# Kernel tuning notes

Measured on AMD Instinct MI355X. Metric: run time of the kernel, lower is better.

## Reference

```python
import jax, jax.numpy as jnp
import numpy as np

B = 64        # graphs per batch
H = 8         # heads
EH = 16       # each_head = ceil(128/8)
HD = 128      # h_dimension
N_DA = 100000
N_Q = 20000
E_DA = 1000000
E_Q = 200000
EPS = 1e-5    # BatchNorm1d eps
SLOPE = 2.0   # leaky_relu_GAT_rate


def setup_inputs() -> dict:
    key = jax.random.key(0)
    ks = jax.random.split(key, 24)
    r = lambda i, shape, s=1.0: jax.random.normal(ks[i], shape, dtype=jnp.float32) * s
    return {
        'h_da_last': r(0, (N_DA, HD)),
        'h_q_last': r(1, (N_Q, HD)),
        'h_da_0': r(2, (N_DA, HD)),
        'h_q_0': r(3, (N_Q, HD)),
        'W_L': r(4, (HD, HD), 0.05), 'b_L': jnp.zeros((HD,), jnp.float32),
        'gateq_W': r(5, (HD, 1), 0.05), 'gateq_b': jnp.zeros((1,), jnp.float32),
        'gate1_W': r(6, (HD, 1), 0.05), 'gate1_b': jnp.zeros((1,), jnp.float32),
        'gate2_W': r(7, (HD, 1), 0.05), 'gate2_b': jnp.zeros((1,), jnp.float32),
        'Q_comb': r(8, (1, HD), 0.1),
        'Qf_W1': r(9, (HD, 2 * HD), 0.05), 'Qf_b1': jnp.zeros((2 * HD,), jnp.float32),
        'Qf_W2': r(10, (2 * HD, 2 * H * EH), 0.05), 'Qf_b2': jnp.zeros((2 * H * EH,), jnp.float32),
        'end_W1': r(11, (H * EH, 2 * HD), 0.05), 'end_b1': jnp.zeros((2 * HD,), jnp.float32),
        'end_W2': r(12, (2 * HD, HD), 0.05), 'end_b2': jnp.zeros((HD,), jnp.float32),
        'src_da': jax.random.randint(ks[13], (E_DA,), 0, N_DA),
        'dst_da': jax.random.randint(ks[14], (E_DA,), 0, N_DA),
        'src_q': jax.random.randint(ks[15], (E_Q,), 0, N_Q),
        'dst_q': jax.random.randint(ks[16], (E_Q,), 0, N_Q),
        'gid_da': jnp.sort(jax.random.randint(ks[17], (N_DA,), 0, B)),
        'gid_q': jnp.sort(jax.random.randint(ks[18], (N_Q,), 0, B)),
        'PEid': jax.random.randint(ks[19], (100000,), 0, E_DA),
        'DEid': jax.random.randint(ks[20], (100000,), 0, E_DA),
        'len_Mn': 5,
    }


def _bn(y):
    # BatchNorm1d(affine=False), training mode: biased batch stats
    mu = jnp.mean(y, axis=0)
    var = jnp.mean((y - mu) ** 2, axis=0)
    return (y - mu) / jnp.sqrt(var + EPS)


def _fnn(x, W1, b1, W2, b2):
    y = jax.nn.elu(_bn(x @ W1 + b1))
    return jax.nn.elu(_bn(y @ W2 + b2))


def _gap(W, b, feat, gid):
    # GlobalAttentionPooling: softmax(gate) over nodes per graph, weighted sum
    g = (feat @ W + b)[:, 0]                               # [N]
    m = jax.ops.segment_max(g, gid, num_segments=B)
    e = jnp.exp(g - m[gid])
    s = jax.ops.segment_sum(e, gid, num_segments=B)
    w = e / s[gid]
    return jax.ops.segment_sum(w[:, None] * feat, gid, num_segments=B)  # [B, HD]


def _edge_softmax(e, dst, n):
    # softmax over incoming edges per destination node, per head. e: [E, H, 1]
    m = jax.ops.segment_max(e, dst, num_segments=n)
    ex = jnp.exp(e - m[dst])
    s = jax.ops.segment_sum(ex, dst, num_segments=n)
    return ex / s[dst]


def forward(h_da_last, h_q_last, h_da_0, h_q_0, W_L, b_L, gateq_W, gateq_b,
            gate1_W, gate1_b, gate2_W, gate2_b, Q_comb, Qf_W1, Qf_b1, Qf_W2, Qf_b2,
            end_W1, end_b1, end_W2, end_b2,
            src_da, dst_da, src_q, dst_q, gid_da, gid_q, PEid, DEid, len_Mn):
    tmp_q = h_q_last  # MM is None branch

    # graph-level query representation -> per-graph attention queries Q [B, H, 2*EH]
    glq = _gap(gateq_W, gateq_b, h_q_last, gid_q)
    Q = _fnn(glq, Qf_W1, Qf_b1, Qf_W2, Qf_b2).reshape(B, H, 2 * EH)

    def att_comb(M1, M2, gid):
        # ATTpolling_for_3Dtensor with shared Q_comb
        k1 = _gap(gate1_W, gate1_b, M1, gid)
        k2 = _gap(gate2_W, gate2_b, M2, gid)
        s = jnp.stack([(Q_comb * k1).sum(-1), (Q_comb * k2).sum(-1)], axis=-1)  # [B, 2]
        a = jax.nn.softmax(s, axis=-1)[gid]                                     # [N, 2]
        return M1 * a[:, 0:1] + M2 * a[:, 1:2]

    def branch(h_last, tmp, h0, M2, src, dst, gid, n):
        Qn = Q[gid]                                  # [n, H, 2*EH]
        Ql, Qr = Qn[..., :EH], Qn[..., EH:]
        feat = (tmp @ W_L + b_L).reshape(n, H, EH)
        el = (feat * Ql).sum(-1, keepdims=True)      # [n, H, 1]
        er = (feat * Qr).sum(-1, keepdims=True)
        fh = att_comb(h0, M2, gid)
        ft = (fh @ W_L + b_L).reshape(n, H, EH)
        e = jax.nn.leaky_relu(el[src] + er[dst], negative_slope=SLOPE)  # [E, H, 1]
        a = _edge_softmax(e, dst, n)
        agg = jax.ops.segment_sum(ft[src] * a, dst, num_segments=n)     # [n, H, EH]
        out = _fnn(agg.reshape(n, H * EH), end_W1, end_b1, end_W2, end_b2)
        return h_last + out, a                       # residual=True

    h_q_next, _ = branch(h_q_last, tmp_q, h_q_0, h_q_last + (h_q_last - tmp_q),
                         src_q, dst_q, gid_q, N_Q)
    h_da_next, a_da = branch(h_da_last, h_da_last, h_da_0, h_da_last,
                             src_da, dst_da, gid_da, N_DA)

    PE = a_da[PEid].sum(axis=0)                      # [H, 1]
    DE = a_da[DEid].sum(axis=0)
    loss = -1.0 * jnp.mean((PE - DE) / len_Mn, axis=0).reshape(1, 1)
    return h_da_next, h_q_next, loss


def reference(h_da_last, h_q_last, h_da_0, h_q_0, W_L, b_L, gateq_W, gateq_b,
              gate1_W, gate1_b, gate2_W, gate2_b, Q_comb, Qf_W1, Qf_b1, Qf_W2, Qf_b2,
              end_W1, end_b1, end_W2, end_b2,
              src_da, dst_da, src_q, dst_q, gid_da, gid_q, PEid, DEid, len_Mn):
    return forward(h_da_last, h_q_last, h_da_0, h_q_0, W_L, b_L, gateq_W, gateq_b,
                   gate1_W, gate1_b, gate2_W, gate2_b, Q_comb, Qf_W1, Qf_b1, Qf_W2, Qf_b2,
                   end_W1, end_b1, end_W2, end_b2,
                   src_da, dst_da, src_q, dst_q, gid_da, gid_q, PEid, DEid, len_Mn)
```

## Files before the change

kernel.cpp:

```cpp
#include <hip/hip_runtime.h>
#include <math.h>

static constexpr int CB   = 64;
static constexpr int CH   = 8;
static constexpr int CEH  = 16;
static constexpr int CHD  = 128;
static constexpr int CNDA = 100000;
static constexpr int CNQ  = 20000;
static constexpr int CEDA = 1000000;
static constexpr int CEQ  = 200000;
static constexpr float CEPS = 1e-5f;
static constexpr float CSLOPE = 2.0f;

typedef unsigned short ushortt;
typedef __attribute__((ext_vector_type(8))) short bf16x8;
typedef __attribute__((ext_vector_type(4))) float f32x4;

__device__ __forceinline__ float ldf(const float* p) { return *p; }
__device__ __forceinline__ float ldf(const ushortt* p) {
  return __uint_as_float(((unsigned)*p) << 16);
}
__device__ __forceinline__ void stf(float* p, float v) { *p = v; }
__device__ __forceinline__ void stf(ushortt* p, float v) {
  unsigned u = __float_as_uint(v);
  u += 0x7fff + ((u >> 16) & 1);
  *p = (ushortt)(u >> 16);
}
__device__ __forceinline__ short f2bf(float v) {
  unsigned u = __float_as_uint(v);
  u += 0x7fff + ((u >> 16) & 1);
  return (short)(u >> 16);
}
__device__ __forceinline__ float bf2f(short b) {
  return __uint_as_float(((unsigned)(ushortt)b) << 16);
}
__device__ __forceinline__ unsigned fenc(float f) {
  unsigned b = __float_as_uint(f);
  return (b & 0x80000000u) ? ~b : (b | 0x80000000u);
}
__device__ __forceinline__ float fdec(unsigned u) {
  unsigned b = (u & 0x80000000u) ? (u ^ 0x80000000u) : ~u;
  return __uint_as_float(b);
}

__global__ void k_zero(float* __restrict__ p, long n) {
  long i = (long)blockIdx.x * blockDim.x + threadIdx.x;
  long stride = (long)gridDim.x * blockDim.x;
  for (; i < n; i += stride) p[i] = 0.f;
}
static inline void zero_launch(void* p, long n, hipStream_t s) {
  long b = (n + 255) / 256;
  int blocks = (int)(b > 4096 ? 4096 : (b < 1 ? 1 : b));
  hipLaunchKernelGGL(k_zero, dim3(blocks), dim3(256), 0, s, (float*)p, n);
}

__global__ void k_binit(int* start, int n) {
  int i = threadIdx.x;
  if (i <= CB) start[i] = n;
}
__global__ void k_bmark(const int* __restrict__ gid, int n, int* __restrict__ start) {
  int i = blockIdx.x * blockDim.x + threadIdx.x;
  if (i >= n) return;
  int g = gid[i];
  if (i == 0 || gid[i - 1] != g) atomicMin(&start[g], i);
}
__global__ void k_bfix(int* start) {
  if (threadIdx.x == 0) {
    for (int g = CB - 1; g >= 0; --g)
      if (start[g] > start[g + 1]) start[g] = start[g + 1];
  }
}

__global__ void k_gate_dot(const float* __restrict__ feat, const float* __restrict__ gw,
                           const float* __restrict__ gb, float* __restrict__ g, int n) {
  int wave = (blockIdx.x * blockDim.x + threadIdx.x) >> 6;
  int lane = threadIdx.x & 63;
  if (wave >= n) return;
  const float* row = feat + (size_t)wave * CHD;
  float v = row[lane] * gw[lane] + row[lane + 64] * gw[lane + 64];
  for (int off = 32; off > 0; off >>= 1) v += __shfl_down(v, off, 64);
  if (lane == 0) g[wave] = v + gb[0];
}

__global__ void k_gate_dot2(const float* __restrict__ feat,
                            const float* __restrict__ w1, const float* __restrict__ b1,
                            const float* __restrict__ w2, const float* __restrict__ b2,
                            float* __restrict__ g1, float* __restrict__ g2, int n) {
  int wave = (blockIdx.x * blockDim.x + threadIdx.x) >> 6;
  int lane = threadIdx.x & 63;
  if (wave >= n) return;
  const float* row = feat + (size_t)wave * CHD;
  float r0 = row[lane], r1 = row[lane + 64];
  float v1 = r0 * w1[lane] + r1 * w1[lane + 64];
  float v2 = r0 * w2[lane] + r1 * w2[lane + 64];
  for (int off = 32; off > 0; off >>= 1) {
    v1 += __shfl_down(v1, off, 64);
    v2 += __shfl_down(v2, off, 64);
  }
  if (lane == 0) {
    g1[wave] = v1 + b1[0];
    g2[wave] = v2 + b2[0];
  }
}

__global__ void k_gmax5(const float* __restrict__ gq, const int* __restrict__ startq,
                        const int* __restrict__ startda, float* __restrict__ m) {
  int job = blockIdx.x >> 6, grp = blockIdx.x & 63;
  const float* g;
  const int* start;
  if (job == 0)      { g = gq;                              start = startq; }
  else if (job == 1) { g = gq + 2 * (size_t)CNQ;            start = startq; }
  else if (job == 2) { g = gq + (size_t)CNQ;                start = startq; }
  else if (job == 3) { g = gq + 3 * (size_t)CNQ;            start = startda; }
  else               { g = gq + 3 * (size_t)CNQ + CNDA;     start = startda; }
  int s0 = start[grp], s1 = start[grp + 1];
  int t = threadIdx.x;
  __shared__ float red[256];
  float v = -1e30f;
  for (int i = s0 + t; i < s1; i += 256) v = fmaxf(v, g[i]);
  red[t] = v;
  __syncthreads();
  for (int o = 128; o > 0; o >>= 1) {
    if (t < o) red[t] = fmaxf(red[t], red[t + o]);
    __syncthreads();
  }
  if (t == 0) m[job * 64 + grp] = red[0];
}

template <int NG>
__global__ __launch_bounds__(128) void k_gap_partial(
    const float* __restrict__ g0, const float* __restrict__ g1,
    const float* __restrict__ feat, const int* __restrict__ start,
    const float* __restrict__ m,
    float* __restrict__ acc0, float* __restrict__ acc1,
    float* __restrict__ sums) {
  int grp = blockIdx.x;
  int s0 = start[grp], s1 = start[grp + 1];
  int len = s1 - s0;
  if (len <= 0) return;
  int NC = gridDim.y;
  int per = (len + NC - 1) / NC;
  int r0 = s0 + blockIdx.y * per;
  int r1 = min(s1, r0 + per);
  if (r0 >= r1) return;
  int t = threadIdx.x;
  float m0 = m[grp];
  float m1 = (NG == 2) ? m[64 + grp] : 0.f;
  float a0 = 0.f, a1 = 0.f, sum0 = 0.f, sum1 = 0.f;
  for (int i = r0; i < r1; ++i) {
    float f = feat[(size_t)i * CHD + t];
    float e0 = __expf(g0[i] - m0);
    sum0 += e0;
    a0 += e0 * f;
    if (NG == 2) {
      float e1 = __expf(g1[i] - m1);
      sum1 += e1;
      a1 += e1 * f;
    }
  }
  atomicAdd(&acc0[grp * CHD + t], a0);
  if (NG == 2) atomicAdd(&acc1[grp * CHD + t], a1);
  if (t == 0) {
    atomicAdd(&sums[grp], sum0);
    if (NG == 2) atomicAdd(&sums[64 + grp], sum1);
  }
}

__global__ void k_gap_norm5(float* __restrict__ glq, const float* __restrict__ sbuf) {
  int job = blockIdx.x >> 6, grp = blockIdx.x & 63;
  int t = threadIdx.x;
  int smap = (job == 1) ? 2 : ((job == 2) ? 1 : job);
  float sv = sbuf[smap * 64 + grp];
  float* acc = glq + (size_t)job * CB * CHD + grp * CHD;
  float v = acc[t];
  acc[t] = (sv > 0.f) ? v / sv : 0.f;
}

__global__ void k_mm_small(const float* __restrict__ X, const float* __restrict__ W,
                           const float* __restrict__ bias, float* __restrict__ Y,
                           int m, int k, int p) {
  int idx = blockIdx.x * blockDim.x + threadIdx.x;
  if (idx >= m * p) return;
  int r = idx / p, c = idx % p;
  const float* xr = X + (size_t)r * k;
  const float* wc = W + c;
  float acc = bias[c];
  int kk = 0;
  for (; kk + 8 <= k; kk += 8) {
    float xv[8], wv[8];
#pragma unroll
    for (int j = 0; j < 8; ++j) {
      xv[j] = xr[kk + j];
      wv[j] = wc[(size_t)(kk + j) * p];
    }
#pragma unroll
    for (int j = 0; j < 8; ++j) acc += xv[j] * wv[j];
  }
  for (; kk < k; ++kk) acc += xr[kk] * wc[(size_t)kk * p];
  Y[idx] = acc;
}

__global__ void k_bn_elu_small(float* __restrict__ Y, int m, int p) {
  int c = blockIdx.x * blockDim.x + threadIdx.x;
  if (c >= p) return;
  float s = 0.f, s2 = 0.f;
  int i = 0;
  for (; i + 8 <= m; i += 8) {
    float v[8];
#pragma unroll
    for (int j = 0; j < 8; ++j) v[j] = Y[(size_t)(i + j) * p + c];
#pragma unroll
    for (int j = 0; j < 8; ++j) { s += v[j]; s2 += v[j] * v[j]; }
  }
  for (; i < m; ++i) {
    float v = Y[(size_t)i * p + c];
    s += v; s2 += v * v;
  }
  float mu = s / m;
  float var = s2 / m - mu * mu;
  float inv = rsqrtf(var + CEPS);
  i = 0;
  for (; i + 8 <= m; i += 8) {
    float v[8];
#pragma unroll
    for (int j = 0; j < 8; ++j) v[j] = Y[(size_t)(i + j) * p + c];
#pragma unroll
    for (int j = 0; j < 8; ++j) {
      float x = (v[j] - mu) * inv;
      Y[(size_t)(i + j) * p + c] = x > 0.f ? x : expm1f(x);
    }
  }
  for (; i < m; ++i) {
    float x = (Y[(size_t)i * p + c] - mu) * inv;
    Y[(size_t)i * p + c] = x > 0.f ? x : expm1f(x);
  }
}

__global__ void k_attcomb(const float* __restrict__ k1, const float* __restrict__ k2,
                          const float* __restrict__ Qc, float* __restrict__ a) {
  int grp = blockIdx.x;
  int t = threadIdx.x;
  float v1 = Qc[t] * k1[grp * CHD + t] + Qc[t + 64] * k1[grp * CHD + t + 64];
  float v2 = Qc[t] * k2[grp * CHD + t] + Qc[t + 64] * k2[grp * CHD + t + 64];
  for (int off = 32; off > 0; off >>= 1) {
    v1 += __shfl_down(v1, off, 64);
    v2 += __shfl_down(v2, off, 64);
  }
  if (t == 0) {
    float mx = fmaxf(v1, v2);
    float e1 = expf(v1 - mx), e2 = expf(v2 - mx);
    float s = e1 + e2;
    a[grp * 2] = e1 / s;
    a[grp * 2 + 1] = e2 / s;
  }
}

__global__ void k_wq(const float* __restrict__ W_L, const float* __restrict__ b_L,
                     const float* __restrict__ Qm, float* __restrict__ WQ,
                     float* __restrict__ bQ) {
  int g = blockIdx.x;
  int t = threadIdx.x;
  for (int j = 0; j < 8; ++j) {
    int idx = t + j * 256;
    int d = idx >> 4, c = idx & 15;
    int h = c & 7, off = (c >= 8) ? CEH : 0;
    const float* w = W_L + d * CHD + h * CEH;
    const float* q = Qm + g * 256 + h * 32 + off;
    float acc = 0.f;
#pragma unroll
    for (int e = 0; e < CEH; ++e) acc += w[e] * q[e];
    WQ[g * 2048 + idx] = acc;
  }
  if (t < 16) {
    int c = t, h = c & 7, off = (c >= 8) ? CEH : 0;
    const float* b = b_L + h * CEH;
    const float* q = Qm + g * 256 + h * 32 + off;
    float acc = 0.f;
#pragma unroll
    for (int e = 0; e < CEH; ++e) acc += b[e] * q[e];
    bQ[g * 16 + c] = acc;
  }
}

__global__ void k_eler(const float* __restrict__ tmp, const float* __restrict__ WQ,
                       const float* __restrict__ bQ, const int* __restrict__ gid,
                       float* __restrict__ elr, int n) {
  int idx = blockIdx.x * blockDim.x + threadIdx.x;
  if (idx >= n * 16) return;
  int i = idx >> 4, c = idx & 15;
  int g = gid[i];
  const float* wq = WQ + g * 2048 + c;
  const float* row = tmp + (size_t)i * CHD;
  float acc = bQ[g * 16 + c];
#pragma unroll 4
  for (int d = 0; d < CHD; ++d) acc += row[d] * wq[d * 16];
  elr[idx] = acc;
}

__global__ void k_elmax(const float* __restrict__ elr, unsigned* __restrict__ mgl, int n) {
  int h = blockIdx.x;
  int chunk = blockIdx.y;
  int per = (n + 31) / 32;
  int i0 = chunk * per, i1 = min(n, i0 + per);
  int t = threadIdx.x;
  __shared__ float red[256];
  float v = -1e30f;
  for (int i = i0 + t; i < i1; i += 256) v = fmaxf(v, elr[(size_t)i * 16 + h]);
  red[t] = v;
  __syncthreads();
  for (int o = 128; o > 0; o >>= 1) {
    if (t < o) red[t] = fmaxf(red[t], red[t + o]);
    __syncthreads();
  }
  if (t == 0) atomicMax(&mgl[h], fenc(red[0]));
}

__global__ void k_tcast(const float* __restrict__ W, ushortt* __restrict__ WT,
                        int K, int P) {
  int i = blockIdx.x * blockDim.x + threadIdx.x;
  if (i >= K * P) return;
  int p = i / K, k = i % K;
  stf(&WT[i], W[(size_t)k * P + p]);
}

template <int P>
__global__ void k_bn_prep(const float* __restrict__ stats, float* __restrict__ pr, int n) {
  int c = threadIdx.x;
  if (c >= P) return;
  float invn = 1.f / (float)n;
  float mu = stats[c] * invn;
  float var = stats[P + c] * invn - mu * mu;
  pr[c] = mu;
  pr[P + c] = rsqrtf(var + CEPS);
}

template <int TP>
__global__ void k_stats_reduce(const float* __restrict__ pstat, float* __restrict__ stats,
                               int nb) {
  int c = blockIdx.x * blockDim.x + threadIdx.x;
  if (c >= TP) return;
  int NC = gridDim.y;
  int per = (nb + NC - 1) / NC;
  int r0 = blockIdx.y * per;
  int r1 = min(nb, r0 + per);
  if (r0 >= r1) return;
  float s0 = 0.f, s1 = 0.f, s2 = 0.f, s3 = 0.f;
  int r = r0;
  for (; r + 4 <= r1; r += 4) {
    s0 += pstat[(size_t)(r + 0) * TP + c];
    s1 += pstat[(size_t)(r + 1) * TP + c];
    s2 += pstat[(size_t)(r + 2) * TP + c];
    s3 += pstat[(size_t)(r + 3) * TP + c];
  }
  for (; r < r1; ++r) s0 += pstat[(size_t)r * TP + c];
  atomicAdd(&stats[c], (s0 + s1) + (s2 + s3));
}

template <int K, int P, int XM, bool STATS, int ROWS, bool LDSB, typename OT>
__global__ __launch_bounds__(256, 2) void k_gemm_mfma(
    const void* __restrict__ X0v, const void* __restrict__ X1v,
    const float* __restrict__ acomb, const int* __restrict__ gid,
    const float* __restrict__ bnpr, const ushortt* __restrict__ BT,
    const float* __restrict__ bias, OT* __restrict__ Y,
    float* __restrict__ pstat, int n) {
  constexpr int NT = P / 16;
  __shared__ ushortt sB[LDSB ? P * K : 1];
  __shared__ float sbn[(XM == 3) ? 2 * K : 1];
  if constexpr (XM == 3) {
    for (int i = threadIdx.x; i < 2 * K; i += 256) sbn[i] = bnpr[i];
  }
  if constexpr (LDSB) {
    for (int i = threadIdx.x; i < P * (K / 8); i += 256) {
      int row = i / (K / 8), seg = i % (K / 8);
      int sseg = seg ^ (row & 7);
      *(bf16x8*)&sB[row * K + sseg * 8] =
          *(const bf16x8*)(BT + (size_t)row * K + seg * 8);
    }
  }
  if constexpr (XM == 3 || LDSB) __syncthreads();
  const int wave = threadIdx.x >> 6, lane = threadIdx.x & 63;
  const int quad = lane >> 4, l16 = lane & 15;
  const int rbase = blockIdx.x * (64 * ROWS) + wave * 16;
  int rA[ROWS];
  bool rok[ROWS];
  float a0[ROWS], a1[ROWS];
#pragma unroll
  for (int rr = 0; rr < ROWS; ++rr) {
    rA[rr] = rbase + rr * 64 + l16;
    rok[rr] = rA[rr] < n;
    a0[rr] = 0.f; a1[rr] = 0.f;
    if (XM == 1 && rok[rr]) {
      int g = gid[rA[rr]];
      a0[rr] = acomb[2 * g];
      a1[rr] = acomb[2 * g + 1];
    }
  }
  f32x4 acc[ROWS][NT];
#pragma unroll
  for (int rr = 0; rr < ROWS; ++rr)
#pragma unroll
    for (int t = 0; t < NT; ++t) acc[rr][t] = f32x4{0.f, 0.f, 0.f, 0.f};
  for (int k0 = 0; k0 < K; k0 += 32) {
    const int kk = k0 + quad * 8;
    bf16x8 af[ROWS];
#pragma unroll
    for (int rr = 0; rr < ROWS; ++rr) {
      af[rr] = bf16x8{};
      if (rok[rr]) {
        if constexpr (XM == 2) {
          af[rr] = *(const bf16x8*)((const ushortt*)X0v + (size_t)rA[rr] * K + kk);
        } else if constexpr (XM == 3) {
          bf16x8 raw = *(const bf16x8*)((const ushortt*)X0v + (size_t)rA[rr] * K + kk);
#pragma unroll
          for (int j = 0; j < 8; ++j) {
            float v = bf2f(raw[j]);
            v = (v - sbn[kk + j]) * sbn[K + kk + j];
            v = v > 0.f ? v : (__expf(v) - 1.f);
            af[rr][j] = f2bf(v);
          }
        } else {
          const float* px = (const float*)X0v + (size_t)rA[rr] * K + kk;
          float v[8];
          if constexpr (XM == 1) {
            const float* py = (const float*)X1v + (size_t)rA[rr] * K + kk;
#pragma unroll
            for (int j = 0; j < 8; ++j) v[j] = a0[rr] * px[j] + a1[rr] * py[j];
          } else {
#pragma unroll
            for (int j = 0; j < 8; ++j) v[j] = px[j];
          }
#pragma unroll
          for (int j = 0; j < 8; ++j) af[rr][j] = f2bf(v[j]);
        }
      }
    }
    bf16x8 bfr[NT];
#pragma unroll
    for (int t = 0; t < NT; ++t) {
      if constexpr (LDSB) {
        int row = t * 16 + l16;
        int sseg = (kk >> 3) ^ (row & 7);
        bfr[t] = *(const bf16x8*)&sB[row * K + sseg * 8];
      } else {
        bfr[t] = *(const bf16x8*)(BT + (size_t)(t * 16 + l16) * K + kk);
      }
    }
#pragma unroll
    for (int rr = 0; rr < ROWS; ++rr)
#pragma unroll
      for (int t = 0; t < NT; ++t)
        acc[rr][t] = __builtin_amdgcn_mfma_f32_16x16x32_bf16(af[rr], bfr[t], acc[rr][t], 0, 0, 0);
  }
  float* pw = nullptr;
  if constexpr (STATS) pw = pstat + ((size_t)blockIdx.x * 4 + wave) * (2 * P);
#pragma unroll
  for (int t = 0; t < NT; ++t) {
    const int c = t * 16 + l16;
    float b = bias[c];
    float s = 0.f, s2 = 0.f;
#pragma unroll
    for (int rr = 0; rr < ROWS; ++rr) {
#pragma unroll
      for (int r = 0; r < 4; ++r) {
        int gr = rbase + rr * 64 + quad * 4 + r;
        if (gr < n) {
          float val = acc[rr][t][r] + b;
          stf(Y + (size_t)gr * P + c, val);
          if constexpr (STATS) {
            float vq = (sizeof(OT) == 2) ? bf2f(f2bf(val)) : val;
            s += vq;
            s2 += vq * vq;
          }
        }
      }
    }
    if constexpr (STATS) {
      s += __shfl_xor(s, 16, 64);
      s += __shfl_xor(s, 32, 64);
      s2 += __shfl_xor(s2, 16, 64);
      s2 += __shfl_xor(s2, 32, 64);
      if (quad == 0) {
        pw[c] = s;
        pw[P + c] = s2;
      }
    }
  }
}

__global__ void k_count(const int* __restrict__ dst, int* __restrict__ counts, int E) {
  int e = blockIdx.x * blockDim.x + threadIdx.x;
  if (e < E) atomicAdd(&counts[dst[e]], 1);
}
__global__ void k_scan_reduce(const int* __restrict__ counts, int* __restrict__ bsum, int n) {
  __shared__ int red[256];
  int t = threadIdx.x;
  int base = blockIdx.x * 1024;
  int s = 0;
  for (int j = 0; j < 4; ++j) {
    int i = base + t * 4 + j;
    if (i < n) s += counts[i];
  }
  red[t] = s;
  __syncthreads();
  for (int o = 128; o > 0; o >>= 1) {
    if (t < o) red[t] += red[t + o];
    __syncthreads();
  }
  if (t == 0) bsum[blockIdx.x] = red[0];
}
__global__ void k_scan_top(int* __restrict__ bsum, int nb) {
  __shared__ int sh[128];
  int t = threadIdx.x;
  int v = (t < nb) ? bsum[t] : 0;
  sh[t] = v;
  __syncthreads();
  for (int o = 1; o < 128; o <<= 1) {
    int x = (t >= o) ? sh[t - o] : 0;
    __syncthreads();
    sh[t] += x;
    __syncthreads();
  }
  if (t < nb) bsum[t] = sh[t] - v;
}
__global__ void k_scan_final(const int* __restrict__ counts, const int* __restrict__ bsum,
                             int* __restrict__ rowptr, int n, int E) {
  __shared__ int sh[256];
  int t = threadIdx.x;
  int base = blockIdx.x * 1024;
  int v[4];
  int s = 0;
  for (int j = 0; j < 4; ++j) {
    int i = base + t * 4 + j;
    v[j] = (i < n) ? counts[i] : 0;
    s += v[j];
  }
  sh[t] = s;
  __syncthreads();
  for (int o = 1; o < 256; o <<= 1) {
    int x = (t >= o) ? sh[t - o] : 0;
    __syncthreads();
    sh[t] += x;
    __syncthreads();
  }
  int off = bsum[blockIdx.x] + sh[t] - s;
  for (int j = 0; j < 4; ++j) {
    int i = base + t * 4 + j;
    if (i < n) rowptr[i] = off;
    off += v[j];
  }
  if (blockIdx.x == 0 && t == 0) rowptr[n] = E;
}
__global__ void k_copy_int(const int* __restrict__ a, int* __restrict__ b, int n) {
  int i = blockIdx.x * blockDim.x + threadIdx.x;
  if (i < n) b[i] = a[i];
}
__global__ void k_scatter(const int* __restrict__ dst, const int* __restrict__ srcA,
                          int* __restrict__ cursor, int* __restrict__ csr_src, int E) {
  int e = blockIdx.x * blockDim.x + threadIdx.x;
  if (e >= E) return;
  int d = dst[e];
  int pos = atomicAdd(&cursor[d], 1);
  csr_src[pos] = srcA[e];
}

__global__ __launch_bounds__(256) void k_node_agg(
    const int* __restrict__ rowptr, const int* __restrict__ csr_src,
    const float* __restrict__ elr, const unsigned* __restrict__ mgl,
    const ushortt* __restrict__ ft,
    float* __restrict__ agg, float* __restrict__ mOut, float* __restrict__ sOut, int n) {
  int node = blockIdx.x * 4 + (threadIdx.x >> 6);
  if (node >= n) return;
  int lane = threadIdx.x & 63;
  int h_p = lane & 7;
  int e_loc = lane >> 3;
  int h_a = lane >> 3;
  int s0 = rowptr[node], s1 = rowptr[node + 1];
  if (s1 <= s0) {
    *(float2*)(agg + (size_t)node * CHD + lane * 2) = make_float2(0.f, 0.f);
    if (lane < 8) {
      mOut[(size_t)node * CH + lane] = -1e30f;
      sOut[(size_t)node * CH + lane] = 0.f;
    }
    return;
  }
  float erd_p = elr[(size_t)node * 16 + 8 + h_p];
  float xm = fdec(mgl[h_p]) + erd_p;
  float m_p = xm >= 0.f ? xm : CSLOPE * xm;
  float s_part = 0.f, a0 = 0.f, a1 = 0.f;
  for (int base = s0; base < s1; base += 8) {
    int cnt = s1 - base;
    int sj = 0;
    float p = 0.f;
    if (e_loc < cnt) {
      sj = csr_src[base + e_loc];
      float x = elr[(size_t)sj * 16 + h_p] + erd_p;
      x = x >= 0.f ? x : CSLOPE * x;
      p = __expf(x - m_p);
      s_part += p;
    }
#pragma unroll
    for (int e = 0; e < 8; ++e) {
      float pe = __shfl(p, e * 8 + h_a, 64);
      int se = __shfl(sj, e * 8, 64);
      unsigned ftv = *(const unsigned*)(ft + (size_t)se * CHD + lane * 2);
      a0 += pe * __uint_as_float(ftv << 16);
      a1 += pe * __uint_as_float(ftv & 0xffff0000u);
    }
  }
  s_part += __shfl_xor(s_part, 8, 64);
  s_part += __shfl_xor(s_part, 16, 64);
  s_part += __shfl_xor(s_part, 32, 64);
  float s_acc = __shfl(s_part, h_a, 64);
  float inv = 1.f / s_acc;
  float2 o;
  o.x = a0 * inv;
  o.y = a1 * inv;
  *(float2*)(agg + (size_t)node * CHD + lane * 2) = o;
  if (lane < 8) {
    mOut[(size_t)node * CH + lane] = m_p;
    sOut[(size_t)node * CH + lane] = s_part;
  }
}

__global__ void k_bn_apply_f4(float* __restrict__ Y, const float* __restrict__ stats,
                              const float* __restrict__ hlast, int n) {
  int idx = blockIdx.x * blockDim.x + threadIdx.x;
  if (idx >= n * 32) return;
  int cg = (idx & 31) * 4;
  float invn = 1.f / (float)n;
  float4 y = ((const float4*)Y)[idx];
  float4 hl = ((const float4*)hlast)[idx];
  float yy[4] = {y.x, y.y, y.z, y.w};
  float hh[4] = {hl.x, hl.y, hl.z, hl.w};
  float o[4];
#pragma unroll
  for (int j = 0; j < 4; ++j) {
    float mu = stats[cg + j] * invn;
    float var = stats[128 + cg + j] * invn - mu * mu;
    float v = (yy[j] - mu) * rsqrtf(var + CEPS);
    v = v > 0.f ? v : (__expf(v) - 1.f);
    o[j] = v + hh[j];
  }
  ((float4*)Y)[idx] = make_float4(o[0], o[1], o[2], o[3]);
}

__device__ __forceinline__ float attn_val(int e, int h, const int* __restrict__ src,
                                          const int* __restrict__ dst,
                                          const float* __restrict__ elr,
                                          const float* __restrict__ mOut,
                                          const float* __restrict__ sOut) {
  int ss = src[e], sd = dst[e];
  float x = elr[(size_t)ss * 16 + h] + elr[(size_t)sd * 16 + 8 + h];
  x = x >= 0.f ? x : CSLOPE * x;
  return __expf(x - mOut[(size_t)sd * CH + h]) / sOut[(size_t)sd * CH + h];
}

__global__ void k_pd(const int* __restrict__ src, const int* __restrict__ dst,
                     const float* __restrict__ elr, const float* __restrict__ mOut,
                     const float* __restrict__ sOut, const int* __restrict__ PEid,
                     const int* __restrict__ DEid, float* __restrict__ pdp,
                     int nPE, int nDE) {
  __shared__ float part[CH];
  if (threadIdx.x < CH) part[threadIdx.x] = 0.f;
  __syncthreads();
  int idx = blockIdx.x * blockDim.x + threadIdx.x;
  int j = idx >> 3, h = idx & 7;
  float acc = 0.f;
  if (j < nPE) acc += attn_val(PEid[j], h, src, dst, elr, mOut, sOut);
  if (j < nDE) acc -= attn_val(DEid[j], h, src, dst, elr, mOut, sOut);
  atomicAdd(&part[h], acc);
  __syncthreads();
  if (threadIdx.x < CH) pdp[(size_t)blockIdx.x * CH + threadIdx.x] = part[threadIdx.x];
}
__global__ void k_loss(const float* __restrict__ pdp, int nb,
                       const int* __restrict__ lenMn, float* __restrict__ out) {
  __shared__ float part[CH];
  int t = threadIdx.x;
  if (t < CH) part[t] = 0.f;
  __syncthreads();
  int h = t & 7;
  float acc = 0.f;
  for (int j = t >> 3; j < nb; j += 32) acc += pdp[(size_t)j * CH + h];
  atomicAdd(&part[h], acc);
  __syncthreads();
  if (t == 0) {
    float len = (float)lenMn[0];
    float s = 0.f;
    for (int hh = 0; hh < CH; ++hh) s += part[hh] / len;
    out[0] = -s / (float)CH;
  }
}

static void run_branch(int n, int E, const float* h_last, const float* h0,
                       const int* src, const int* dst, const int* gid,
                       const float* acomb, const float* WQ, const float* bQ,
                       const ushortt* W_LT, const float* b_L,
                       const ushortt* W1T, const float* end_b1,
                       const ushortt* W2T, const float* end_b2,
                       float* U, float* elr, unsigned* mgl, float* mOut, float* sOut,
                       int* counts, int* rowptr, int* cursor, int* csr_src, int* bsum,
                       float* stats ,
                       float* bnpr , float* pstat, float* out, hipStream_t stream) {
  ushortt* ftB = (ushortt*)U;
  ushortt* y1B = (ushortt*)U;
  float* stats1 = stats;
  float* stats2 = stats + 512;
  int nChunks = (n + 1023) / 1024;
  int nbG1 = (n + 127) / 128;
  int nbG2 = (n + 63) / 64;
  zero_launch(counts, n, stream);
  zero_launch(stats, 1024, stream);
  zero_launch(mgl, 8, stream);
  hipLaunchKernelGGL(k_count, dim3((E + 255) / 256), dim3(256), 0, stream, dst, counts, E);
  hipLaunchKernelGGL(k_scan_reduce, dim3(nChunks), dim3(256), 0, stream, counts, bsum, n);
  hipLaunchKernelGGL(k_scan_top, dim3(1), dim3(128), 0, stream, bsum, nChunks);
  hipLaunchKernelGGL(k_scan_final, dim3(nChunks), dim3(256), 0, stream, counts, bsum, rowptr, n, E);
  hipLaunchKernelGGL(k_copy_int, dim3((n + 255) / 256), dim3(256), 0, stream, rowptr, cursor, n);
  hipLaunchKernelGGL(k_scatter, dim3((E + 255) / 256), dim3(256), 0, stream, dst, src, cursor, csr_src, E);
  hipLaunchKernelGGL(k_eler, dim3((n * 16 + 255) / 256), dim3(256), 0, stream,
                     h_last, WQ, bQ, gid, elr, n);
  hipLaunchKernelGGL(k_elmax, dim3(8, 32), dim3(256), 0, stream, elr, mgl, n);
  hipLaunchKernelGGL((k_gemm_mfma<128, 128, 1, false, 2, false, ushortt>), dim3(nbG1),
                     dim3(256), 0, stream, h0, h_last, acomb, gid,
                     (const float*)nullptr, W_LT, b_L, ftB, (float*)nullptr, n);
  hipLaunchKernelGGL(k_node_agg, dim3((n + 3) / 4), dim3(256), 0, stream,
                     rowptr, csr_src, elr, mgl, ftB, out, mOut, sOut, n);
  hipLaunchKernelGGL((k_gemm_mfma<128, 256, 0, true, 1, true, ushortt>), dim3(nbG2),
                     dim3(256), 0, stream, out, (const void*)nullptr,
                     (const float*)nullptr, (const int*)nullptr,
                     (const float*)nullptr, W1T, end_b1, y1B, pstat, n);
  hipLaunchKernelGGL((k_stats_reduce<512>), dim3(2, 64), dim3(256), 0, stream,
                     pstat, stats1, nbG2 * 4);
  hipLaunchKernelGGL((k_bn_prep<256>), dim3(1), dim3(256), 0, stream, stats1, bnpr, n);
  hipLaunchKernelGGL((k_gemm_mfma<256, 128, 3, true, 2, false, float>), dim3(nbG1),
                     dim3(256), 0, stream, y1B, (const void*)nullptr,
                     (const float*)nullptr, (const int*)nullptr,
                     bnpr, W2T, end_b2, out, pstat, n);
  hipLaunchKernelGGL((k_stats_reduce<256>), dim3(1, 64), dim3(256), 0, stream,
                     pstat, stats2, nbG1 * 4);
  hipLaunchKernelGGL(k_bn_apply_f4, dim3((n * 32 + 255) / 256), dim3(256), 0, stream,
                     out, stats2, h_last, n);
}

extern "C" void kernel_launch(void* const* d_in, const int* in_sizes, int n_in,
                              void* d_out, int out_size, void* d_ws, size_t ws_size,
                              hipStream_t stream) {
  const float* h_da_last = (const float*)d_in[0];
  const float* h_q_last  = (const float*)d_in[1];
  const float* h_da_0    = (const float*)d_in[2];
  const float* h_q_0     = (const float*)d_in[3];
  const float* W_L       = (const float*)d_in[4];
  const float* b_L       = (const float*)d_in[5];
  const float* gateq_W   = (const float*)d_in[6];
  const float* gateq_b   = (const float*)d_in[7];
  const float* gate1_W   = (const float*)d_in[8];
  const float* gate1_b   = (const float*)d_in[9];
  const float* gate2_W   = (const float*)d_in[10];
  const float* gate2_b   = (const float*)d_in[11];
  const float* Q_comb    = (const float*)d_in[12];
  const float* Qf_W1     = (const float*)d_in[13];
  const float* Qf_b1     = (const float*)d_in[14];
  const float* Qf_W2     = (const float*)d_in[15];
  const float* Qf_b2     = (const float*)d_in[16];
  const float* end_W1    = (const float*)d_in[17];
  const float* end_b1    = (const float*)d_in[18];
  const float* end_W2    = (const float*)d_in[19];
  const float* end_b2    = (const float*)d_in[20];
  const int* src_da = (const int*)d_in[21];
  const int* dst_da = (const int*)d_in[22];
  const int* src_q  = (const int*)d_in[23];
  const int* dst_q  = (const int*)d_in[24];
  const int* gid_da = (const int*)d_in[25];
  const int* gid_q  = (const int*)d_in[26];
  const int* PEid   = (const int*)d_in[27];
  const int* DEid   = (const int*)d_in[28];
  const int* len_Mn = (const int*)d_in[29];

  float* out_da   = (float*)d_out;
  float* out_q    = (float*)d_out + (size_t)CNDA * CHD;
  float* out_loss = (float*)d_out + (size_t)CNDA * CHD + (size_t)CNQ * CHD;

  float* ws = (float*)d_ws;
  size_t off = 0;
  auto alloc = [&](size_t cnt) { float* p = ws + off; off += cnt; return p; };
  float* U    = alloc((size_t)CNDA * 128);
  float* elr  = alloc((size_t)CNDA * 16);
  float* mOut = alloc((size_t)CNDA * CH);
  float* sOut = alloc((size_t)CNDA * CH);
  int* counts  = (int*)alloc(CNDA);
  int* rowptr  = (int*)alloc(CNDA + 4);
  int* cursor  = (int*)alloc(CNDA);
  int* csr_src = (int*)alloc(CEDA);
  int* bsum    = (int*)alloc(128);
  ushortt* W_LT = (ushortt*)alloc(128 * 128 / 2);
  ushortt* W1T  = (ushortt*)alloc(128 * 256 / 2);
  ushortt* W2T  = (ushortt*)alloc(256 * 128 / 2);
  float* WQ   = alloc((size_t)CB * 2048);
  float* bQ   = alloc((size_t)CB * 16);
  float* gq   = alloc(CNQ);
  float* g1q  = alloc(CNQ);
  float* g2q  = alloc(CNQ);
  float* g1da = alloc(CNDA);
  float* g2da = alloc(CNDA);
  float* glq  = alloc(CB * CHD);
  float* k1q  = alloc(CB * CHD);
  float* k2q  = alloc(CB * CHD);
  float* k1da = alloc(CB * CHD);
  float* k2da = alloc(CB * CHD);
  float* Qt   = alloc(CB * 256);
  float* Qm   = alloc(CB * 256);
  float* acq  = alloc(CB * 2);
  float* acda = alloc(CB * 2);
  float* stats = alloc(1024);
  float* bnpr  = alloc(512);
  unsigned* mgl = (unsigned*)alloc(8);
  float* mbuf  = alloc(5 * 64);
  float* sbuf  = alloc(5 * 64);
  int* startq  = (int*)alloc(68);
  int* startda = (int*)alloc(68);
  float* pstat = alloc(((size_t)(CNDA + 63) / 64) * 4 * 512);
  float* pdp   = alloc(((size_t)CNDA * CH + 255) / 256 * CH);
  (void)ws_size; (void)n_in; (void)out_size;

  hipLaunchKernelGGL(k_tcast, dim3((128 * 128 + 255) / 256), dim3(256), 0, stream, W_L, W_LT, 128, 128);
  hipLaunchKernelGGL(k_tcast, dim3((128 * 256 + 255) / 256), dim3(256), 0, stream, end_W1, W1T, 128, 256);
  hipLaunchKernelGGL(k_tcast, dim3((256 * 128 + 255) / 256), dim3(256), 0, stream, end_W2, W2T, 256, 128);

  hipLaunchKernelGGL(k_binit, dim3(1), dim3(128), 0, stream, startq, CNQ);
  hipLaunchKernelGGL(k_binit, dim3(1), dim3(128), 0, stream, startda, CNDA);
  hipLaunchKernelGGL(k_bmark, dim3((CNQ + 255) / 256), dim3(256), 0, stream, gid_q, CNQ, startq);
  hipLaunchKernelGGL(k_bmark, dim3((CNDA + 255) / 256), dim3(256), 0, stream, gid_da, CNDA, startda);
  hipLaunchKernelGGL(k_bfix, dim3(1), dim3(64), 0, stream, startq);
  hipLaunchKernelGGL(k_bfix, dim3(1), dim3(64), 0, stream, startda);

  hipLaunchKernelGGL(k_gate_dot2, dim3((CNQ + 3) / 4), dim3(256), 0, stream,
                     h_q_last, gateq_W, gateq_b, gate2_W, gate2_b, gq, g2q, CNQ);
  hipLaunchKernelGGL(k_gate_dot, dim3((CNQ + 3) / 4), dim3(256), 0, stream, h_q_0, gate1_W, gate1_b, g1q, CNQ);
  hipLaunchKernelGGL(k_gate_dot, dim3((CNDA + 3) / 4), dim3(256), 0, stream, h_da_0, gate1_W, gate1_b, g1da, CNDA);
  hipLaunchKernelGGL(k_gate_dot, dim3((CNDA + 3) / 4), dim3(256), 0, stream, h_da_last, gate2_W, gate2_b, g2da, CNDA);

  hipLaunchKernelGGL(k_gmax5, dim3(5 * CB), dim3(256), 0, stream, gq, startq, startda, mbuf);
  zero_launch(glq, 5 * (size_t)CB * CHD, stream);
  zero_launch(sbuf, 5 * 64, stream);
  hipLaunchKernelGGL((k_gap_partial<2>), dim3(CB, 32), dim3(128), 0, stream,
                     gq, g2q, h_q_last, startq, mbuf + 0, glq, k2q, sbuf + 0);
  hipLaunchKernelGGL((k_gap_partial<1>), dim3(CB, 32), dim3(128), 0, stream,
                     g1q, (const float*)nullptr, h_q_0, startq, mbuf + 128,
                     k1q, (float*)nullptr, sbuf + 128);
  hipLaunchKernelGGL((k_gap_partial<1>), dim3(CB, 32), dim3(128), 0, stream,
                     g1da, (const float*)nullptr, h_da_0, startda, mbuf + 192,
                     k1da, (float*)nullptr, sbuf + 192);
  hipLaunchKernelGGL((k_gap_partial<1>), dim3(CB, 32), dim3(128), 0, stream,
                     g2da, (const float*)nullptr, h_da_last, startda, mbuf + 256,
                     k2da, (float*)nullptr, sbuf + 256);
  hipLaunchKernelGGL(k_gap_norm5, dim3(5 * CB), dim3(128), 0, stream, glq, sbuf);

  hipLaunchKernelGGL(k_mm_small, dim3((CB * 256 + 255) / 256), dim3(256), 0, stream,
                     glq, Qf_W1, Qf_b1, Qt, CB, 128, 256);
  hipLaunchKernelGGL(k_bn_elu_small, dim3(1), dim3(256), 0, stream, Qt, CB, 256);
  hipLaunchKernelGGL(k_mm_small, dim3((CB * 256 + 255) / 256), dim3(256), 0, stream,
                     Qt, Qf_W2, Qf_b2, Qm, CB, 256, 256);
  hipLaunchKernelGGL(k_bn_elu_small, dim3(1), dim3(256), 0, stream, Qm, CB, 256);

  hipLaunchKernelGGL(k_wq, dim3(CB), dim3(256), 0, stream, W_L, b_L, Qm, WQ, bQ);

  hipLaunchKernelGGL(k_attcomb, dim3(CB), dim3(64), 0, stream, k1q, k2q, Q_comb, acq);
  hipLaunchKernelGGL(k_attcomb, dim3(CB), dim3(64), 0, stream, k1da, k2da, Q_comb, acda);

  run_branch(CNQ, CEQ, h_q_last, h_q_0, src_q, dst_q, gid_q, acq, WQ, bQ,
             W_LT, b_L, W1T, end_b1, W2T, end_b2,
             U, elr, mgl, mOut, sOut, counts, rowptr, cursor, csr_src, bsum,
             stats, bnpr, pstat, out_q, stream);

  run_branch(CNDA, CEDA, h_da_last, h_da_0, src_da, dst_da, gid_da, acda, WQ, bQ,
             W_LT, b_L, W1T, end_b1, W2T, end_b2,
             U, elr, mgl, mOut, sOut, counts, rowptr, cursor, csr_src, bsum,
             stats, bnpr, pstat, out_da, stream);

  int nPE = in_sizes[27], nDE = in_sizes[28];
  int nMax = nPE > nDE ? nPE : nDE;
  int nbPD = (nMax * CH + 255) / 256;
  hipLaunchKernelGGL(k_pd, dim3(nbPD), dim3(256), 0, stream,
                     src_da, dst_da, elr, mOut, sOut, PEid, DEid, pdp, nPE, nDE);
  hipLaunchKernelGGL(k_loss, dim3(1), dim3(256), 0, stream, pdp, nbPD, len_Mn, out_loss);
}
```

Baseline: 1.070 ms.

## Prefetch A fragments before B staging and store B in fragment-major LDS layout

```diff
diff --git a/kernel.cpp b/kernel.cpp
--- a/kernel.cpp
+++ b/kernel.cpp
@@ -366,18 +366,6 @@
   constexpr int NT = P / 16;
   __shared__ ushortt sB[LDSB ? P * K : 1];
   __shared__ float sbn[(XM == 3) ? 2 * K : 1];
-  if constexpr (XM == 3) {
-    for (int i = threadIdx.x; i < 2 * K; i += 256) sbn[i] = bnpr[i];
-  }
-  if constexpr (LDSB) {
-    for (int i = threadIdx.x; i < P * (K / 8); i += 256) {
-      int row = i / (K / 8), seg = i % (K / 8);
-      int sseg = seg ^ (row & 7);
-      *(bf16x8*)&sB[row * K + sseg * 8] =
-          *(const bf16x8*)(BT + (size_t)row * K + seg * 8);
-    }
-  }
-  if constexpr (XM == 3 || LDSB) __syncthreads();
   const int wave = threadIdx.x >> 6, lane = threadIdx.x & 63;
   const int quad = lane >> 4, l16 = lane & 15;
   const int rbase = blockIdx.x * (64 * ROWS) + wave * 16;
@@ -395,6 +383,36 @@
       a1[rr] = acomb[2 * g + 1];
     }
   }
+  bf16x8 afp[LDSB ? (K / 32) : 1];
+  if constexpr (LDSB) {
+    if (rok[0]) {
+#pragma unroll
+      for (int ks = 0; ks < K / 32; ++ks) {
+        const float* px = (const float*)X0v + (size_t)rA[0] * K + ks * 32 + quad * 8;
+        float v[8];
+#pragma unroll
+        for (int j = 0; j < 8; ++j) v[j] = px[j];
+#pragma unroll
+        for (int j = 0; j < 8; ++j) afp[ks][j] = f2bf(v[j]);
+      }
+    } else {
+#pragma unroll
+      for (int ks = 0; ks < K / 32; ++ks) afp[ks] = bf16x8{};
+    }
+  }
+  if constexpr (XM == 3) {
+    for (int i = threadIdx.x; i < 2 * K; i += 256) sbn[i] = bnpr[i];
+  }
+  if constexpr (LDSB) {
+    constexpr int SEGS = K / 8;
+    for (int i = threadIdx.x; i < P * SEGS; i += 256) {
+      int row = i / SEGS, seg = i % SEGS;
+      int ks = seg >> 2, qd = seg & 3, tt = row >> 4, ll = row & 15;
+      int frag = ((ks * NT + tt) * 64 + qd * 16 + ll) ^ (seg & 7);
+      *(bf16x8*)&sB[frag * 8] = *(const bf16x8*)(BT + (size_t)row * K + seg * 8);
+    }
+  }
+  if constexpr (XM == 3 || LDSB) __syncthreads();
   f32x4 acc[ROWS][NT];
 #pragma unroll
   for (int rr = 0; rr < ROWS; ++rr)
@@ -403,34 +421,38 @@
   for (int k0 = 0; k0 < K; k0 += 32) {
     const int kk = k0 + quad * 8;
     bf16x8 af[ROWS];
-#pragma unroll
-    for (int rr = 0; rr < ROWS; ++rr) {
-      af[rr] = bf16x8{};
-      if (rok[rr]) {
-        if constexpr (XM == 2) {
-          af[rr] = *(const bf16x8*)((const ushortt*)X0v + (size_t)rA[rr] * K + kk);
-        } else if constexpr (XM == 3) {
-          bf16x8 raw = *(const bf16x8*)((const ushortt*)X0v + (size_t)rA[rr] * K + kk);
-#pragma unroll
-          for (int j = 0; j < 8; ++j) {
-            float v = bf2f(raw[j]);
-            v = (v - sbn[kk + j]) * sbn[K + kk + j];
-            v = v > 0.f ? v : (__expf(v) - 1.f);
-            af[rr][j] = f2bf(v);
+    if constexpr (LDSB) {
+      af[0] = afp[k0 >> 5];
+    } else {
+#pragma unroll
+      for (int rr = 0; rr < ROWS; ++rr) {
+        af[rr] = bf16x8{};
+        if (rok[rr]) {
+          if constexpr (XM == 2) {
+            af[rr] = *(const bf16x8*)((const ushortt*)X0v + (size_t)rA[rr] * K + kk);
+          } else if constexpr (XM == 3) {
+            bf16x8 raw = *(const bf16x8*)((const ushortt*)X0v + (size_t)rA[rr] * K + kk);
+#pragma unroll
+            for (int j = 0; j < 8; ++j) {
+              float v = bf2f(raw[j]);
+              v = (v - sbn[kk + j]) * sbn[K + kk + j];
+              v = v > 0.f ? v : (__expf(v) - 1.f);
+              af[rr][j] = f2bf(v);
+            }
+          } else {
+            const float* px = (const float*)X0v + (size_t)rA[rr] * K + kk;
+            float v[8];
+            if constexpr (XM == 1) {
+              const float* py = (const float*)X1v + (size_t)rA[rr] * K + kk;
+#pragma unroll
+              for (int j = 0; j < 8; ++j) v[j] = a0[rr] * px[j] + a1[rr] * py[j];
+            } else {
+#pragma unroll
+              for (int j = 0; j < 8; ++j) v[j] = px[j];
+            }
+#pragma unroll
+            for (int j = 0; j < 8; ++j) af[rr][j] = f2bf(v[j]);
           }
-        } else {
-          const float* px = (const float*)X0v + (size_t)rA[rr] * K + kk;
-          float v[8];
-          if constexpr (XM == 1) {
-            const float* py = (const float*)X1v + (size_t)rA[rr] * K + kk;
-#pragma unroll
-            for (int j = 0; j < 8; ++j) v[j] = a0[rr] * px[j] + a1[rr] * py[j];
-          } else {
-#pragma unroll
-            for (int j = 0; j < 8; ++j) v[j] = px[j];
-          }
-#pragma unroll
-          for (int j = 0; j < 8; ++j) af[rr][j] = f2bf(v[j]);
         }
       }
     }
@@ -438,9 +460,9 @@
 #pragma unroll
     for (int t = 0; t < NT; ++t) {
       if constexpr (LDSB) {
-        int row = t * 16 + l16;
-        int sseg = (kk >> 3) ^ (row & 7);
-        bfr[t] = *(const bf16x8*)&sB[row * K + sseg * 8];
+        int ks = k0 >> 5;
+        int frag = ((ks * NT + t) * 64 + lane) ^ ((ks * 4 + quad) & 7);
+        bfr[t] = *(const bf16x8*)&sB[frag * 8];
       } else {
         bfr[t] = *(const bf16x8*)(BT + (size_t)(t * 16 + l16) * K + kk);
       }
```

Measured after the change: 1.078 ms. No clear change (+0.7%).
